# Performance work log

Hardware: AMD Instinct MI355X
Metric: run time of the kernel (lower is better)

## Reference

```python
import jax, jax.numpy as jnp
import numpy as np

B, S, C, L = 8, 256, 4, 256
E, H, NL, NS = 256, 8, 2, 8
DH = E // H
EPS = 1e-5


def _conv1d(x, w, b):
    # x: [B, Cin, L], w: [Cout, Cin, K] -> [B, Cout, L] (SAME padding, stride 1)
    y = jax.lax.conv_general_dilated(x, w, (1,), 'SAME', dimension_numbers=('NCH', 'OIH', 'NCH'))
    return y + b[None, :, None]


def _local_cnn(xs, w1, b1, w2, b2):
    # xs: [B, 4, L] for one segment; per-segment weights
    h = jax.nn.relu(_conv1d(xs, w1, b1))
    h = jax.nn.relu(_conv1d(h, w2, b2))
    return jnp.max(h, axis=-1)  # AdaptiveMaxPool1d(1) + squeeze -> [B, E]


def _layernorm(x, g, b):
    m = jnp.mean(x, axis=-1, keepdims=True)
    v = jnp.mean((x - m) ** 2, axis=-1, keepdims=True)
    return (x - m) / jnp.sqrt(v + EPS) * g + b


def setup_inputs() -> dict:
    key = jax.random.key(0)
    ks = jax.random.split(key, 24)
    n = lambda k, shp, s: jax.random.normal(k, shp, jnp.float32) * s
    return {
        'x': jax.random.normal(ks[0], (B, S, C, L), jnp.float32),
        'conv1_w': n(ks[1], (S, 128, 4, 3), 0.1), 'conv1_b': jnp.zeros((S, 128), jnp.float32),
        'conv2_w': n(ks[2], (S, E, 128, 3), 0.05), 'conv2_b': jnp.zeros((S, E), jnp.float32),
        'ln1_g': jnp.ones((NL, E), jnp.float32), 'ln1_b': jnp.zeros((NL, E), jnp.float32),
        'wq': n(ks[3], (NL, E, E), 0.02), 'bq': jnp.zeros((NL, E), jnp.float32),
        'wk': n(ks[4], (NL, E, E), 0.02), 'bk': jnp.zeros((NL, E), jnp.float32),
        'wv': n(ks[5], (NL, E, E), 0.02), 'bv': jnp.zeros((NL, E), jnp.float32),
        'wo': n(ks[6], (NL, E, E), 0.02), 'bo': jnp.zeros((NL, E), jnp.float32),
        'bias_w': n(ks[7], (NL, 4, H), 0.1), 'bias_b': jnp.zeros((NL, H), jnp.float32),
        'ln2_g': jnp.ones((NL, E), jnp.float32), 'ln2_b': jnp.zeros((NL, E), jnp.float32),
        'ffn_w1': n(ks[8], (NL, E, 2 * E), 0.02), 'ffn_b1': jnp.zeros((NL, 2 * E), jnp.float32),
        'ffn_w2': n(ks[9], (NL, 2 * E, E), 0.02), 'ffn_b2': jnp.zeros((NL, E), jnp.float32),
        'fc_w': n(ks[10], (NS * E, 2), 0.02), 'fc_b': jnp.zeros((2,), jnp.float32),
    }


def _forward(x, conv1_w, conv1_b, conv2_w, conv2_b, ln1_g, ln1_b,
             wq, bq, wk, bk, wv, bv, wo, bo, bias_w, bias_b,
             ln2_g, ln2_b, ffn_w1, ffn_b1, ffn_w2, ffn_b2, fc_w, fc_b):
    # Per-segment CNNs (vmap over segment axis with per-segment weights) -> [B, S, E]
    cnn = jax.vmap(_local_cnn, in_axes=(1, 0, 0, 0, 0), out_axes=1)(x, conv1_w, conv1_b, conv2_w, conv2_b)
    feat = _layernorm(cnn, jnp.ones((E,), cnn.dtype), jnp.zeros((E,), cnn.dtype))  # F.layer_norm, no affine

    # bias matrices: cdist (p=2), global-max normalized; positional distance; inverses
    sq = jnp.sum(feat * feat, axis=-1)  # [B, S]
    d2 = sq[:, :, None] + sq[:, None, :] - 2.0 * jnp.einsum('bie,bje->bij', feat, feat)
    dist = jnp.sqrt(jnp.maximum(d2, 0.0))
    dist = dist / (jnp.max(dist) + 1e-6)
    idx = jnp.arange(S, dtype=feat.dtype)
    rdist = jnp.abs(idx[:, None] - idx[None, :]) / (S - 1)
    rdist = jnp.broadcast_to(rdist[None], (feat.shape[0], S, S))
    attn_bias = jnp.stack([dist, rdist, 1.0 - rdist, 1.0 - dist], axis=-1)  # [B,S,S,4]

    h = feat
    scale = 1.0 / jnp.sqrt(jnp.asarray(DH, h.dtype))
    for l in range(NL):
        hn = _layernorm(h, ln1_g[l], ln1_b[l])
        q = (hn @ wq[l] + bq[l]).reshape(-1, S, H, DH)
        k = (hn @ wk[l] + bk[l]).reshape(-1, S, H, DH)
        v = (hn @ wv[l] + bv[l]).reshape(-1, S, H, DH)
        scores = jnp.einsum('bihd,bjhd->bhij', q, k) * scale
        scores = scores + jnp.einsum('bijc,ch->bhij', attn_bias, bias_w[l]) + bias_b[l][None, :, None, None]
        a = jax.nn.softmax(scores, axis=-1)
        o = jnp.einsum('bhij,bjhd->bihd', a, v).reshape(-1, S, E) @ wo[l] + bo[l]
        h = h + o
        hn2 = _layernorm(h, ln2_g[l], ln2_b[l])
        f = jax.nn.relu(hn2 @ ffn_w1[l] + ffn_b1[l]) @ ffn_w2[l] + ffn_b2[l]
        h = h + f

    # split into NS chunks along segments, max-pool each, concat (S % NS == 0)
    pooled = jnp.max(h.reshape(-1, NS, S // NS, E), axis=2).reshape(-1, NS * E)
    return pooled @ fc_w + fc_b  # [B, num_classes]


def reference(x, conv1_w, conv1_b, conv2_w, conv2_b, ln1_g, ln1_b,
              wq, bq, wk, bk, wv, bv, wo, bo, bias_w, bias_b,
              ln2_g, ln2_b, ffn_w1, ffn_b1, ffn_w2, ffn_b2, fc_w, fc_b):
    return _forward(x, conv1_w, conv1_b, conv2_w, conv2_b, ln1_g, ln1_b,
                    wq, bq, wk, bk, wv, bv, wo, bo, bias_w, bias_b,
                    ln2_g, ln2_b, ffn_w1, ffn_b1, ffn_w2, ffn_b2, fc_w, fc_b)
```

## Files before the change

### kernel.cpp

```cpp
#include <hip/hip_runtime.h>
#include <hip/hip_bf16.h>


typedef float floatx4 __attribute__((ext_vector_type(4)));
typedef short bf16x8 __attribute__((ext_vector_type(8)));

__device__ __forceinline__ float wave_sum(float v) {
    v += __shfl_xor(v, 32); v += __shfl_xor(v, 16); v += __shfl_xor(v, 8);
    v += __shfl_xor(v, 4);  v += __shfl_xor(v, 2);  v += __shfl_xor(v, 1);
    return v;
}
__device__ __forceinline__ float wave_max(float v) {
    v = fmaxf(v, __shfl_xor(v, 32)); v = fmaxf(v, __shfl_xor(v, 16));
    v = fmaxf(v, __shfl_xor(v, 8));  v = fmaxf(v, __shfl_xor(v, 4));
    v = fmaxf(v, __shfl_xor(v, 2));  v = fmaxf(v, __shfl_xor(v, 1));
    return v;
}
__device__ __forceinline__ unsigned short f2bf(float v) {
    unsigned b = __float_as_uint(v);
    unsigned r = (b + 0x7fffu + ((b >> 16) & 1u)) >> 16;
    return (unsigned short)r;
}

typedef const __attribute__((address_space(1))) unsigned int* gas_u32p;
typedef __attribute__((address_space(3))) unsigned int* las_u32p;

__device__ __forceinline__ void stage_chunk(const unsigned short* gbase,
                                            unsigned short* lbase,
                                            int wv, int lane)
{
    const char* g = (const char*)gbase + (wv << 11) + (lane << 4);
    char* l = (char*)lbase + (wv << 11);
    __builtin_amdgcn_global_load_lds((gas_u32p)(const void*)g,
                                     (las_u32p)(void*)l, 16, 0, 0);
    __builtin_amdgcn_global_load_lds((gas_u32p)(const void*)(g + 1024),
                                     (las_u32p)(void*)(l + 1024), 16, 0, 0);
}

__global__ __launch_bounds__(256) void prep_all_kernel(
    unsigned* __restrict__ dmax, unsigned* __restrict__ cnnmax,
    const float* __restrict__ wq, const float* __restrict__ wk,
    const float* __restrict__ wv, const float* __restrict__ wo,
    const float* __restrict__ f1, const float* __restrict__ f2,
    unsigned short* __restrict__ wtb,
    const float* __restrict__ w2, unsigned short* __restrict__ w2b)
{
    __shared__ float t[32][33];
    const int bid = blockIdx.x;
    const int tid = threadIdx.x;

    if (bid < 2048) {
        const size_t i = (size_t)bid * 256 + tid;
        cnnmax[i] = 0u;
        if (i == 0) *dmax = 0u;
        return;
    }
    if (bid < 5120) {
        const int idx = bid - 2048;
        const int z = idx >> 8;
        const int by = (idx >> 4) & 15;
        const int bx = idx & 15;
        const int l = z / 6, id = z % 6;
        const float* src; int K_, N_; size_t doff;
        switch (id) {
            case 0:  src = wq + (size_t)l * 65536;  K_ = 256; N_ = 256; doff = 0;      break;
            case 1:  src = wk + (size_t)l * 65536;  K_ = 256; N_ = 256; doff = 65536;  break;
            case 2:  src = wv + (size_t)l * 65536;  K_ = 256; N_ = 256; doff = 131072; break;
            case 3:  src = wo + (size_t)l * 65536;  K_ = 256; N_ = 256; doff = 196608; break;
            case 4:  src = f1 + (size_t)l * 131072; K_ = 256; N_ = 512; doff = 262144; break;
            default: src = f2 + (size_t)l * 131072; K_ = 512; N_ = 256; doff = 393216; break;
        }
        const int k0 = bx * 32, n0 = by * 32;
        if (k0 >= K_ || n0 >= N_) return;
        unsigned short* dst = wtb + (size_t)l * 524288 + doff;
        const int c = tid & 31, rq = tid >> 5;
#pragma unroll
        for (int i = 0; i < 4; i++) {
            const int r = rq + i * 8;
            t[r][c] = src[(size_t)(k0 + r) * N_ + n0 + c];
        }
        __syncthreads();
#pragma unroll
        for (int i = 0; i < 4; i++) {
            const int r = rq + i * 8;
            dst[(size_t)(n0 + r) * K_ + k0 + c] = f2bf(t[c][r]);
        }
        return;
    }
    {
        const int idx = bid - 5120;
        const int s = idx & 255;
        const int part = idx >> 8;
        const float* src = w2 + (size_t)s * 98304;
        unsigned short* dst = w2b + (size_t)s * 98304;
        for (int o = part * 24576 + tid; o < (part + 1) * 24576; o += 256) {
            const int c  = o >> 13;
            const int w  = o & 8191;
            const int co = w >> 5;
            const int up = (w >> 3) & 3;
            const int tt = w & 7;
            const int u  = (up ^ co ^ (co >> 2)) & 3;
            const int kk = c * 32 + u * 8 + tt;
            const int ci = kk & 127, tap = kk >> 7;
            dst[o] = f2bf(src[(size_t)co * 384 + ci * 3 + tap]);
        }
    }
}

__global__ __launch_bounds__(512, 4) void conv2_fused_kernel(
    const unsigned short* __restrict__ w2b,
    const float* __restrict__ x,
    const float* __restrict__ w1,
    const float* __restrict__ b1,
    const float* __restrict__ b2,
    unsigned* __restrict__ cnnmax)
{
    __shared__ float xs[4][258];
    __shared__ float w1s[1536];
    __shared__ unsigned short Hs[130 * 136];
    __shared__ unsigned short Ab[2][8192];

    const int tid = threadIdx.x;
    const int lane = tid & 63;
    const int wv = __builtin_amdgcn_readfirstlane((int)(tid >> 6));
    const int wm = wv & 3, wn = wv >> 2;
    const int bid = blockIdx.x;
    const int xcd = bid & 7;
    const int pos = bid >> 3;
    const int s   = xcd * 32 + (pos >> 4);
    const int nt  = pos & 15;
    const int b = nt >> 1;
    const int l0 = (nt & 1) * 128;
    const int lr = lane & 15;
    const int quad = lane >> 4;
    const int qk = quad * 8;

    const float* xp = x + ((size_t)(b * 256 + s)) * 1024;
    for (int i = tid; i < 1024; i += 512) {
        const int ci = i >> 8, l = i & 255;
        xs[ci][l + 1] = xp[i];
    }
    if (tid < 4) { xs[tid][0] = 0.f; xs[tid][257] = 0.f; }
    const float* w1p = w1 + (size_t)s * 1536;
    for (int i = tid; i < 1536; i += 512) w1s[i] = w1p[i];
    const int co1 = tid & 127;
    const float bb1 = b1[s * 128 + co1];
    __syncthreads();

    const unsigned short* wchunks = w2b + (size_t)s * 98304;
    stage_chunk(wchunks, &Ab[0][0], wv, lane);

    {
        const int g = tid >> 7;
        float wreg[12];
#pragma unroll
        for (int k = 0; k < 12; k++) wreg[k] = w1s[co1 * 12 + k];
        for (int pr = g; pr < 130; pr += 4) {
            const int l = l0 - 1 + pr;
            float a = 0.f;
            if ((unsigned)l < 256u) {
                a = bb1;
#pragma unroll
                for (int ci = 0; ci < 4; ci++)
#pragma unroll
                    for (int k = 0; k < 3; k++) a = fmaf(wreg[ci * 3 + k], xs[ci][l + k], a);
                a = fmaxf(a, 0.f);
            }
            Hs[pr * 136 + co1] = f2bf(a);
        }
    }

    floatx4 acc[4][4];
#pragma unroll
    for (int r = 0; r < 4; r++)
#pragma unroll
        for (int c = 0; c < 4; c++) acc[r][c] = (floatx4){0.f, 0.f, 0.f, 0.f};

    const int nb = wn * 64;
    const int aoff = wm * 2048 + lr * 32 + (((quad ^ lr ^ (lr >> 2)) & 3) * 8);
    const int hbase = (nb + lr) * 136 + qk;

    asm volatile("s_waitcnt vmcnt(0) lgkmcnt(0)" ::: "memory");
    __builtin_amdgcn_s_barrier();
    __builtin_amdgcn_sched_barrier(0);

#pragma unroll
    for (int ks = 0; ks < 12; ks++) {
        if (ks) {
            asm volatile("s_waitcnt vmcnt(0)" ::: "memory");
            __builtin_amdgcn_s_barrier();
            __builtin_amdgcn_sched_barrier(0);
        }
        if (ks < 11)
            stage_chunk(wchunks + (size_t)(ks + 1) * 8192, &Ab[(ks + 1) & 1][0], wv, lane);
        const int tap_ = ks >> 2, ci0_ = (ks & 3) * 32;
        const unsigned short* ap = &Ab[ks & 1][aoff];
        const unsigned short* hp = &Hs[hbase + tap_ * 136 + ci0_];
        bf16x8 a[4], bb[4];
#pragma unroll
        for (int r = 0; r < 4; r++) a[r] = *(const bf16x8*)(ap + r * 512);
#pragma unroll
        for (int c = 0; c < 4; c++) bb[c] = *(const bf16x8*)(hp + c * 2176);
#pragma unroll
        for (int r = 0; r < 4; r++)
#pragma unroll
            for (int c = 0; c < 4; c++)
                acc[r][c] = __builtin_amdgcn_mfma_f32_16x16x32_bf16(
                    a[r], bb[c], acc[r][c], 0, 0, 0);
    }

    const float* b2s = b2 + s * 256;
    unsigned* cmrow = cnnmax + ((size_t)(b * 256 + s)) * 256;
#pragma unroll
    for (int r = 0; r < 4; r++) {
#pragma unroll
        for (int e = 0; e < 4; e++) {
            const int co = wm * 64 + r * 16 + quad * 4 + e;
            const float bias = b2s[co];
            float mv = 0.f;
#pragma unroll
            for (int c = 0; c < 4; c++) mv = fmaxf(mv, acc[r][c][e] + bias);
            mv = fmaxf(mv, __shfl_xor(mv, 1));
            mv = fmaxf(mv, __shfl_xor(mv, 2));
            mv = fmaxf(mv, __shfl_xor(mv, 4));
            mv = fmaxf(mv, __shfl_xor(mv, 8));
            if (lr == 0) atomicMax(&cmrow[co], __float_as_uint(mv));
        }
    }
}

__global__ __launch_bounds__(256) void ln0_kernel(
    const unsigned* __restrict__ cm, float* __restrict__ out, float* __restrict__ sqv)
{
    const int tid = threadIdx.x, lane = tid & 63, wid = tid >> 6;
    const int row = blockIdx.x * 4 + wid;
    const unsigned* xr = cm + (size_t)row * 256;
    float v[4];
#pragma unroll
    for (int i = 0; i < 4; i++) v[i] = __uint_as_float(xr[lane + 64 * i]);
    float sm = wave_sum(v[0] + v[1] + v[2] + v[3]);
    const float mean = sm * (1.f / 256.f);
    float qv = 0.f;
#pragma unroll
    for (int i = 0; i < 4; i++) { const float d = v[i] - mean; qv = fmaf(d, d, qv); }
    qv = wave_sum(qv);
    const float inv = rsqrtf(qv * (1.f / 256.f) + 1e-5f);
    float* orow = out + (size_t)row * 256;
#pragma unroll
    for (int i = 0; i < 4; i++) orow[lane + 64 * i] = (v[i] - mean) * inv;
    if (lane == 0) sqv[row] = qv * inv * inv;
}

__global__ __launch_bounds__(256) void dist_kernel(
    const float* __restrict__ feat, const float* __restrict__ sq,
    float* __restrict__ dist, unsigned* __restrict__ dmax)
{
    __shared__ float Fi[32][260];
    __shared__ float Fj[16][260];
    __shared__ float redm[4];
    const int tid = threadIdx.x;
    const int bid = blockIdx.x;
    const int b = bid >> 7, it = (bid >> 4) & 7, jt = bid & 15;
    const float* fb = feat + (size_t)b * 65536;
    for (int idx = tid; idx < 32 * 256; idx += 256) {
        const int r = idx >> 8, e = idx & 255;
        Fi[r][e] = fb[(it * 32 + r) * 256 + e];
    }
    for (int idx = tid; idx < 16 * 256; idx += 256) {
        const int r = idx >> 8, e = idx & 255;
        Fj[r][e] = fb[(jt * 16 + r) * 256 + e];
    }
    __syncthreads();
    const int ii = tid >> 3, j0 = (tid & 7) * 2;
    float acc[2] = {0.f, 0.f};
    for (int e = 0; e < 256; e += 4) {
        const float4 a = *(const float4*)&Fi[ii][e];
#pragma unroll
        for (int u = 0; u < 2; u++) {
            const float4 bv = *(const float4*)&Fj[j0 + u][e];
            acc[u] += a.x * bv.x + a.y * bv.y + a.z * bv.z + a.w * bv.w;
        }
    }
    const float sqi = sq[b * 256 + it * 32 + ii];
    float mymax = 0.f;
#pragma unroll
    for (int u = 0; u < 2; u++) {
        const float d2 = sqi + sq[b * 256 + jt * 16 + j0 + u] - 2.f * acc[u];
        const float d = sqrtf(fmaxf(d2, 0.f));
        dist[((size_t)b * 256 + it * 32 + ii) * 256 + jt * 16 + j0 + u] = d;
        mymax = fmaxf(mymax, d);
    }
    mymax = wave_max(mymax);
    if ((tid & 63) == 0) redm[tid >> 6] = mymax;
    __syncthreads();
    if (tid == 0) {
        const float m = fmaxf(fmaxf(redm[0], redm[1]), fmaxf(redm[2], redm[3]));
        atomicMax(dmax, __float_as_uint(m));
    }
}

__global__ __launch_bounds__(128) void gemm_ln_kernel(
    const float* __restrict__ hf, const unsigned short* __restrict__ Wt,
    const float* __restrict__ g, const float* __restrict__ bta,
    const float* __restrict__ b0, const float* __restrict__ b1, const float* __restrict__ b2,
    unsigned short* __restrict__ o0, unsigned short* __restrict__ o1, unsigned short* __restrict__ o2,
    int mode)
{
    __shared__ unsigned short As[64 * 264];
    const int tid = threadIdx.x;
    const int lane = tid & 63, lr = lane & 15, quad = lane >> 4;
    const int wv = __builtin_amdgcn_readfirstlane((int)(tid >> 6));
    const int m0 = blockIdx.x * 64;
    const int n0 = blockIdx.y * 32;

    {
        const int g16 = lane >> 4, l16 = lane & 15;
        const int c0 = l16 * 16;
        float4 g4[4], bt4[4];
#pragma unroll
        for (int k = 0; k < 4; k++) {
            g4[k]  = *(const float4*)&g[c0 + 4 * k];
            bt4[k] = *(const float4*)&bta[c0 + 4 * k];
        }
#pragma unroll
        for (int pass = 0; pass < 8; pass++) {
            const int row = wv * 32 + pass * 4 + g16;
            const float* hr = hf + (size_t)(m0 + row) * 256 + c0;
            float4 v[4];
#pragma unroll
            for (int k = 0; k < 4; k++) v[k] = *(const float4*)&hr[4 * k];
            float s = 0.f;
#pragma unroll
            for (int k = 0; k < 4; k++) s += v[k].x + v[k].y + v[k].z + v[k].w;
            s += __shfl_xor(s, 1); s += __shfl_xor(s, 2);
            s += __shfl_xor(s, 4); s += __shfl_xor(s, 8);
            const float mean = s * (1.f / 256.f);
            float q = 0.f;
#pragma unroll
            for (int k = 0; k < 4; k++) {
                float d;
                d = v[k].x - mean; q = fmaf(d, d, q);
                d = v[k].y - mean; q = fmaf(d, d, q);
                d = v[k].z - mean; q = fmaf(d, d, q);
                d = v[k].w - mean; q = fmaf(d, d, q);
            }
            q += __shfl_xor(q, 1); q += __shfl_xor(q, 2);
            q += __shfl_xor(q, 4); q += __shfl_xor(q, 8);
            const float inv = rsqrtf(q * (1.f / 256.f) + 1e-5f);
            unsigned* dst = (unsigned*)&As[row * 264 + c0];
#pragma unroll
            for (int k = 0; k < 4; k++) {
                const float f0 = (v[k].x - mean) * inv * g4[k].x + bt4[k].x;
                const float f1 = (v[k].y - mean) * inv * g4[k].y + bt4[k].y;
                const float f2 = (v[k].z - mean) * inv * g4[k].z + bt4[k].z;
                const float f3 = (v[k].w - mean) * inv * g4[k].w + bt4[k].w;
                dst[2 * k]     = (unsigned)f2bf(f0) | ((unsigned)f2bf(f1) << 16);
                dst[2 * k + 1] = (unsigned)f2bf(f2) | ((unsigned)f2bf(f3) << 16);
            }
        }
    }
    __syncthreads();

    floatx4 acc[2][2];
#pragma unroll
    for (int r = 0; r < 2; r++)
#pragma unroll
        for (int c = 0; c < 2; c++) acc[r][c] = (floatx4){0.f, 0.f, 0.f, 0.f};

    const unsigned short* Ap = &As[(wv * 32 + lr) * 264 + quad * 8];
    const unsigned short* Bp = Wt + (size_t)(n0 + lr) * 256 + quad * 8;
#pragma unroll
    for (int ks = 0; ks < 8; ks++) {
        const int ko = ks * 32;
        bf16x8 a[2], b[2];
#pragma unroll
        for (int r = 0; r < 2; r++) a[r] = *(const bf16x8*)(Ap + r * 16 * 264 + ko);
#pragma unroll
        for (int c = 0; c < 2; c++) b[c] = *(const bf16x8*)(Bp + (size_t)c * 16 * 256 + ko);
#pragma unroll
        for (int r = 0; r < 2; r++)
#pragma unroll
            for (int c = 0; c < 2; c++)
                acc[r][c] = __builtin_amdgcn_mfma_f32_16x16x32_bf16(a[r], b[c], acc[r][c], 0, 0, 0);
    }

    const int mw0 = m0 + wv * 32;
    if (mode == 0) {
        const int which = n0 >> 8, nn0 = n0 & 255;
        if (which < 2) {
            unsigned short* op = which ? o1 : o0;
            const float* bp = which ? b1 : b0;
#pragma unroll
            for (int r = 0; r < 2; r++)
#pragma unroll
                for (int c = 0; c < 2; c++)
#pragma unroll
                    for (int e = 0; e < 4; e++) {
                        const int m = mw0 + r * 16 + quad * 4 + e;
                        const int n = nn0 + c * 16 + lr;
                        op[(size_t)m * 256 + n] = f2bf(acc[r][c][e] + bp[n]);
                    }
        } else {
#pragma unroll
            for (int r = 0; r < 2; r++)
#pragma unroll
                for (int c = 0; c < 2; c++)
#pragma unroll
                    for (int e = 0; e < 4; e++) {
                        const int m = mw0 + r * 16 + quad * 4 + e;
                        const int nn = nn0 + c * 16 + lr;
                        const int bb_ = m >> 8, j = m & 255, hh = nn >> 5, d = nn & 31;
                        o2[(size_t)((bb_ * 8 + hh) * 32 + d) * 256 + j] = f2bf(acc[r][c][e] + b2[nn]);
                    }
        }
    } else {
#pragma unroll
        for (int r = 0; r < 2; r++)
#pragma unroll
            for (int c = 0; c < 2; c++)
#pragma unroll
                for (int e = 0; e < 4; e++) {
                    const int m = mw0 + r * 16 + quad * 4 + e;
                    const int n = n0 + c * 16 + lr;
                    o0[(size_t)m * 512 + n] = f2bf(fmaxf(acc[r][c][e] + b0[n], 0.f));
                }
    }
}

__global__ __launch_bounds__(128) void gemm_mfma_kernel(
    const unsigned short* __restrict__ A, const unsigned short* __restrict__ Wt,
    const float* __restrict__ b0, const float* __restrict__ b1, const float* __restrict__ b2,
    const float* __restrict__ R, float* __restrict__ outf,
    unsigned short* __restrict__ o0, unsigned short* __restrict__ o1, unsigned short* __restrict__ o2,
    int K, int mode)
{
    const int tid = threadIdx.x;
    const int lane = tid & 63, lr = lane & 15, quad = lane >> 4;
    const int wv = __builtin_amdgcn_readfirstlane((int)(tid >> 6));
    const int m0 = blockIdx.x * 64 + wv * 32;
    const int n0 = blockIdx.y * 32;

    floatx4 acc[2][2];
#pragma unroll
    for (int r = 0; r < 2; r++)
#pragma unroll
        for (int c = 0; c < 2; c++) acc[r][c] = (floatx4){0.f, 0.f, 0.f, 0.f};

    const unsigned short* Ap = A + (size_t)(m0 + lr) * K + quad * 8;
    const unsigned short* Bp = Wt + (size_t)(n0 + lr) * K + quad * 8;
    const int nks = K >> 5;
#pragma unroll 4
    for (int ks = 0; ks < nks; ks++) {
        const int ko = ks * 32;
        bf16x8 a[2], b[2];
#pragma unroll
        for (int r = 0; r < 2; r++) a[r] = *(const bf16x8*)(Ap + (size_t)r * 16 * K + ko);
#pragma unroll
        for (int c = 0; c < 2; c++) b[c] = *(const bf16x8*)(Bp + (size_t)c * 16 * K + ko);
#pragma unroll
        for (int r = 0; r < 2; r++)
#pragma unroll
            for (int c = 0; c < 2; c++)
                acc[r][c] = __builtin_amdgcn_mfma_f32_16x16x32_bf16(a[r], b[c], acc[r][c], 0, 0, 0);
    }

    if (mode == 0) {
        const int which = n0 >> 8, nn0 = n0 & 255;
        if (which < 2) {
            unsigned short* op = which ? o1 : o0;
            const float* bp = which ? b1 : b0;
#pragma unroll
            for (int r = 0; r < 2; r++)
#pragma unroll
                for (int c = 0; c < 2; c++)
#pragma unroll
                    for (int e = 0; e < 4; e++) {
                        const int m = m0 + r * 16 + quad * 4 + e;
                        const int n = nn0 + c * 16 + lr;
                        op[(size_t)m * 256 + n] = f2bf(acc[r][c][e] + bp[n]);
                    }
        } else {
#pragma unroll
            for (int r = 0; r < 2; r++)
#pragma unroll
                for (int c = 0; c < 2; c++)
#pragma unroll
                    for (int e = 0; e < 4; e++) {
                        const int m = m0 + r * 16 + quad * 4 + e;
                        const int nn = nn0 + c * 16 + lr;
                        const int bb_ = m >> 8, j = m & 255, hh = nn >> 5, d = nn & 31;
                        o2[(size_t)((bb_ * 8 + hh) * 32 + d) * 256 + j] = f2bf(acc[r][c][e] + b2[nn]);
                    }
        }
    } else if (mode == 1) {
#pragma unroll
        for (int r = 0; r < 2; r++)
#pragma unroll
            for (int c = 0; c < 2; c++)
#pragma unroll
                for (int e = 0; e < 4; e++) {
                    const int m = m0 + r * 16 + quad * 4 + e;
                    const int n = n0 + c * 16 + lr;
                    outf[(size_t)m * 256 + n] = acc[r][c][e] + b0[n] + R[(size_t)m * 256 + n];
                }
    } else {
#pragma unroll
        for (int r = 0; r < 2; r++)
#pragma unroll
            for (int c = 0; c < 2; c++)
#pragma unroll
                for (int e = 0; e < 4; e++) {
                    const int m = m0 + r * 16 + quad * 4 + e;
                    const int n = n0 + c * 16 + lr;
                    o0[(size_t)m * 512 + n] = f2bf(fmaxf(acc[r][c][e] + b0[n], 0.f));
                }
    }
}

__global__ __launch_bounds__(256) void attn_mfma_kernel(
    const unsigned short* __restrict__ q_bf, const unsigned short* __restrict__ k_bf,
    const unsigned short* __restrict__ vt_bf,
    const float* __restrict__ dist, const unsigned* __restrict__ dmax,
    const float* __restrict__ bw, const float* __restrict__ bb,
    unsigned short* __restrict__ ao_bf)
{
    __shared__ unsigned short Ps[4][16][264];
    const int tid = threadIdx.x;
    const int lane = tid & 63, lr = lane & 15, quad = lane >> 4;
    const int wv = __builtin_amdgcn_readfirstlane((int)(tid >> 6));
    const int ic = blockIdx.x, hh = blockIdx.y, b = blockIdx.z;
    const int i0 = ic * 64 + wv * 16;

    const float dinv = 1.f / (__uint_as_float(*dmax) + 1e-6f);
    const float w0 = bw[0 * 8 + hh], w1 = bw[1 * 8 + hh], w2 = bw[2 * 8 + hh], w3 = bw[3 * 8 + hh];
    const float bbh = bb[hh];
    const float scale = 0.17677669529663687f;

    const bf16x8 aq = *(const bf16x8*)(q_bf + (size_t)(b * 256 + i0 + lr) * 256 + hh * 32 + quad * 8);
    floatx4 sc[16];
#pragma unroll
    for (int c = 0; c < 16; c++) {
        const bf16x8 bk = *(const bf16x8*)(k_bf + (size_t)(b * 256 + c * 16 + lr) * 256 + hh * 32 + quad * 8);
        sc[c] = __builtin_amdgcn_mfma_f32_16x16x32_bf16(aq, bk, (floatx4){0.f, 0.f, 0.f, 0.f}, 0, 0, 0);
    }

#pragma unroll
    for (int e = 0; e < 4; e++) {
        const int i = i0 + quad * 4 + e;
        const float* drow = dist + ((size_t)(b * 256 + i)) * 256;
        float bs[16];
        float mx = -1e30f;
#pragma unroll
        for (int c = 0; c < 16; c++) {
            const int j = c * 16 + lr;
            const float dn = drow[j] * dinv;
            const float rd = fabsf((float)(i - j)) * (1.f / 255.f);
            bs[c] = sc[c][e] * scale + w0 * dn + w1 * rd + w2 * (1.f - rd) + w3 * (1.f - dn) + bbh;
            mx = fmaxf(mx, bs[c]);
        }
        mx = fmaxf(mx, __shfl_xor(mx, 1)); mx = fmaxf(mx, __shfl_xor(mx, 2));
        mx = fmaxf(mx, __shfl_xor(mx, 4)); mx = fmaxf(mx, __shfl_xor(mx, 8));
        float sm = 0.f;
#pragma unroll
        for (int c = 0; c < 16; c++) { bs[c] = __expf(bs[c] - mx); sm += bs[c]; }
        sm += __shfl_xor(sm, 1); sm += __shfl_xor(sm, 2);
        sm += __shfl_xor(sm, 4); sm += __shfl_xor(sm, 8);
        const float rs = 1.f / sm;
#pragma unroll
        for (int c = 0; c < 16; c++)
            Ps[wv][quad * 4 + e][c * 16 + lr] = f2bf(bs[c] * rs);
    }
    __syncthreads();

    floatx4 oc[2];
    oc[0] = (floatx4){0.f, 0.f, 0.f, 0.f};
    oc[1] = (floatx4){0.f, 0.f, 0.f, 0.f};
    const unsigned short* vtb = vt_bf + (size_t)(b * 8 + hh) * 8192;
#pragma unroll
    for (int ks = 0; ks < 8; ks++) {
        const bf16x8 ap = *(const bf16x8*)(&Ps[wv][lr][ks * 32 + quad * 8]);
#pragma unroll
        for (int c2 = 0; c2 < 2; c2++) {
            const bf16x8 bvv = *(const bf16x8*)(vtb + (size_t)(c2 * 16 + lr) * 256 + ks * 32 + quad * 8);
            oc[c2] = __builtin_amdgcn_mfma_f32_16x16x32_bf16(ap, bvv, oc[c2], 0, 0, 0);
        }
    }
#pragma unroll
    for (int c2 = 0; c2 < 2; c2++)
#pragma unroll
        for (int e = 0; e < 4; e++)
            ao_bf[(size_t)(b * 256 + i0 + quad * 4 + e) * 256 + hh * 32 + c2 * 16 + lr] = f2bf(oc[c2][e]);
}

__global__ __launch_bounds__(256) void pool_fc_kernel(
    const float* __restrict__ h, const float* __restrict__ fcw,
    const float* __restrict__ fcb, float* __restrict__ out)
{
    __shared__ float red[8];
    const int b = blockIdx.x, tid = threadIdx.x, lane = tid & 63, wid = tid >> 6;
    float a0 = 0.f, a1 = 0.f;
    for (int ns = 0; ns < 8; ns++) {
        const float* hp = h + ((size_t)(b * 256 + ns * 32)) * 256 + tid;
        float m = hp[0];
#pragma unroll
        for (int r = 1; r < 32; r++) m = fmaxf(m, hp[(size_t)r * 256]);
        a0 = fmaf(m, fcw[(ns * 256 + tid) * 2 + 0], a0);
        a1 = fmaf(m, fcw[(ns * 256 + tid) * 2 + 1], a1);
    }
    a0 = wave_sum(a0);
    a1 = wave_sum(a1);
    if (lane == 0) { red[wid] = a0; red[4 + wid] = a1; }
    __syncthreads();
    if (tid == 0) out[b * 2 + 0] = red[0] + red[1] + red[2] + red[3] + fcb[0];
    if (tid == 1) out[b * 2 + 1] = red[4] + red[5] + red[6] + red[7] + fcb[1];
}

extern "C" void kernel_launch(void* const* d_in, const int* in_sizes, int n_in,
                              void* d_out, int out_size, void* d_ws, size_t ws_size,
                              hipStream_t stream)
{
    (void)in_sizes; (void)n_in; (void)out_size; (void)ws_size;
    const float* x       = (const float*)d_in[0];
    const float* conv1_w = (const float*)d_in[1];
    const float* conv1_b = (const float*)d_in[2];
    const float* conv2_w = (const float*)d_in[3];
    const float* conv2_b = (const float*)d_in[4];
    const float* ln1_g   = (const float*)d_in[5];
    const float* ln1_b   = (const float*)d_in[6];
    const float* wq = (const float*)d_in[7];  const float* bq = (const float*)d_in[8];
    const float* wk = (const float*)d_in[9];  const float* bk = (const float*)d_in[10];
    const float* wvp = (const float*)d_in[11]; const float* bv = (const float*)d_in[12];
    const float* wo = (const float*)d_in[13]; const float* bo = (const float*)d_in[14];
    const float* bias_w = (const float*)d_in[15];
    const float* bias_b = (const float*)d_in[16];
    const float* ln2_g  = (const float*)d_in[17];
    const float* ln2_b  = (const float*)d_in[18];
    const float* ffn_w1 = (const float*)d_in[19]; const float* ffn_b1 = (const float*)d_in[20];
    const float* ffn_w2 = (const float*)d_in[21]; const float* ffn_b2 = (const float*)d_in[22];
    const float* fc_w   = (const float*)d_in[23]; const float* fc_b = (const float*)d_in[24];
    float* out = (float*)d_out;

    float* ws = (float*)d_ws;
    float* h    = ws;
    float* dist = h + 524288;
    float* sqv  = dist + 524288;
    unsigned* dmax = (unsigned*)(sqv + 2048);
    unsigned* cnnmax = (unsigned*)(sqv + 2048 + 16);
    unsigned short* hn_bf = (unsigned short*)(sqv + 2048 + 16 + 524288);
    unsigned short* q_bf  = hn_bf + 524288;
    unsigned short* k_bf  = q_bf + 524288;
    unsigned short* vt_bf = k_bf + 524288;
    unsigned short* ao_bf = vt_bf + 524288;
    unsigned short* fm_bf = ao_bf + 524288;
    unsigned short* wtb   = fm_bf + 1048576;
    unsigned short* w2b   = wtb + 1048576;

    prep_all_kernel<<<6144, 256, 0, stream>>>(
        dmax, cnnmax, wq, wk, wvp, wo, ffn_w1, ffn_w2, wtb, conv2_w, w2b);
    conv2_fused_kernel<<<4096, 512, 0, stream>>>(
        w2b, x, conv1_w, conv1_b, conv2_b, cnnmax);
    ln0_kernel<<<512, 256, 0, stream>>>(cnnmax, h, sqv);
    dist_kernel<<<1024, 256, 0, stream>>>(h, sqv, dist, dmax);

    for (int l = 0; l < 2; l++) {
        const unsigned short* wqkvT = wtb + (size_t)l * 524288;
        const unsigned short* woT   = wqkvT + 196608;
        const unsigned short* f1T   = wqkvT + 262144;
        const unsigned short* f2T   = wqkvT + 393216;

        gemm_ln_kernel<<<dim3(32, 24), 128, 0, stream>>>(
            h, wqkvT, ln1_g + l * 256, ln1_b + l * 256,
            bq + l * 256, bk + l * 256, bv + l * 256,
            q_bf, k_bf, vt_bf, 0);
        attn_mfma_kernel<<<dim3(4, 8, 8), 256, 0, stream>>>(
            q_bf, k_bf, vt_bf, dist, dmax, bias_w + l * 32, bias_b + l * 8, ao_bf);
        gemm_mfma_kernel<<<dim3(32, 8), 128, 0, stream>>>(
            ao_bf, woT, bo + l * 256, nullptr, nullptr,
            h, h, nullptr, nullptr, nullptr, 256, 1);
        gemm_ln_kernel<<<dim3(32, 16), 128, 0, stream>>>(
            h, f1T, ln2_g + l * 256, ln2_b + l * 256,
            ffn_b1 + l * 512, nullptr, nullptr,
            fm_bf, nullptr, nullptr, 2);
        gemm_mfma_kernel<<<dim3(32, 8), 128, 0, stream>>>(
            fm_bf, f2T, ffn_b2 + l * 256, nullptr, nullptr,
            h, h, nullptr, nullptr, nullptr, 512, 1);
    }
    pool_fc_kernel<<<8, 256, 0, stream>>>(h, fc_w, fc_b, out);
}
```

Measured before the change: 571.9 us.

## Vectorize conv2 weight prep, pack conv1 outputs in pairs, split pool-fc across segments

The conv2 weight conversion now reads float4s coalesced from the source and scatters them to the swizzled bf16 layout through a per-block LDS index table, instead of doing a gathered scalar read per output element. Conv1 in the fused kernel now computes two output channels per thread with packed 2-wide FMAs and writes both bf16 values in one 32-bit store. The pool_fc kernel is spread over 64 blocks, one per batch and chunk, and accumulates into the output with atomicAdd. The output is pre-initialised with the fc bias inside the prep kernel. This adds float atomics, so the summation order is no longer deterministic.

Measured after the change: 575.3 us. Within noise of the previous version (+0.6%).

```diff
diff --git a/kernel.cpp b/kernel.cpp
--- a/kernel.cpp
+++ b/kernel.cpp
@@ -3,6 +3,7 @@
 
 
 typedef float floatx4 __attribute__((ext_vector_type(4)));
+typedef float f32x2 __attribute__((ext_vector_type(2)));
 typedef short bf16x8 __attribute__((ext_vector_type(8)));
 
 __device__ __forceinline__ float wave_sum(float v) {
@@ -43,9 +44,11 @@
     const float* __restrict__ wv, const float* __restrict__ wo,
     const float* __restrict__ f1, const float* __restrict__ f2,
     unsigned short* __restrict__ wtb,
-    const float* __restrict__ w2, unsigned short* __restrict__ w2b)
+    const float* __restrict__ w2, unsigned short* __restrict__ w2b,
+    const float* __restrict__ fcb, float* __restrict__ outbuf)
 {
     __shared__ float t[32][33];
+    __shared__ unsigned tbl[1536];
     const int bid = blockIdx.x;
     const int tid = threadIdx.x;
 
@@ -53,6 +56,7 @@
         const size_t i = (size_t)bid * 256 + tid;
         cnnmax[i] = 0u;
         if (i == 0) *dmax = 0u;
+        if (bid == 0 && tid < 16) outbuf[tid] = fcb[tid & 1];
         return;
     }
     if (bid < 5120) {
@@ -91,18 +95,29 @@
         const int idx = bid - 5120;
         const int s = idx & 255;
         const int part = idx >> 8;
-        const float* src = w2 + (size_t)s * 98304;
+        for (int i = tid; i < 1536; i += 256) {
+            const int sw = i / 384, j = i - sw * 384;
+            const int ci = (j * 21846) >> 16;
+            const int tap = j - ci * 3;
+            const int kk = tap * 128 + ci;
+            const int c = kk >> 5, rel = kk & 31;
+            const int u = rel >> 3, tt = rel & 7;
+            tbl[i] = (unsigned)(c * 8192 + (((u ^ sw) & 3) << 3) + tt);
+        }
+        __syncthreads();
+        const float4* src4 = (const float4*)(w2 + (size_t)s * 98304);
         unsigned short* dst = w2b + (size_t)s * 98304;
-        for (int o = part * 24576 + tid; o < (part + 1) * 24576; o += 256) {
-            const int c  = o >> 13;
-            const int w  = o & 8191;
-            const int co = w >> 5;
-            const int up = (w >> 3) & 3;
-            const int tt = w & 7;
-            const int u  = (up ^ co ^ (co >> 2)) & 3;
-            const int kk = c * 32 + u * 8 + tt;
-            const int ci = kk & 127, tap = kk >> 7;
-            dst[o] = f2bf(src[(size_t)co * 384 + ci * 3 + tap]);
+        for (int q = part * 6144 + tid; q < (part + 1) * 6144; q += 256) {
+            const int co = (((q >> 5) * 21846) >> 16);
+            const int j0 = (q - co * 96) * 4;
+            const int sw = (co ^ (co >> 2)) & 3;
+            const unsigned* tb = &tbl[sw * 384 + j0];
+            const float4 v = src4[q];
+            const int base = co * 32;
+            dst[tb[0] + base] = f2bf(v.x);
+            dst[tb[1] + base] = f2bf(v.y);
+            dst[tb[2] + base] = f2bf(v.z);
+            dst[tb[3] + base] = f2bf(v.w);
         }
     }
 }
@@ -143,30 +158,35 @@
     if (tid < 4) { xs[tid][0] = 0.f; xs[tid][257] = 0.f; }
     const float* w1p = w1 + (size_t)s * 1536;
     for (int i = tid; i < 1536; i += 512) w1s[i] = w1p[i];
-    const int co1 = tid & 127;
-    const float bb1 = b1[s * 128 + co1];
+    const int co2 = (tid & 63) * 2;
+    const f32x2 bb2 = {b1[s * 128 + co2], b1[s * 128 + co2 + 1]};
     __syncthreads();
 
     const unsigned short* wchunks = w2b + (size_t)s * 98304;
     stage_chunk(wchunks, &Ab[0][0], wv, lane);
 
     {
-        const int g = tid >> 7;
-        float wreg[12];
-#pragma unroll
-        for (int k = 0; k < 12; k++) wreg[k] = w1s[co1 * 12 + k];
-        for (int pr = g; pr < 130; pr += 4) {
+        const int g8 = tid >> 6;
+        f32x2 wreg[12];
+#pragma unroll
+        for (int k = 0; k < 12; k++)
+            wreg[k] = (f32x2){w1s[co2 * 12 + k], w1s[co2 * 12 + 12 + k]};
+        for (int pr = g8; pr < 130; pr += 8) {
             const int l = l0 - 1 + pr;
-            float a = 0.f;
+            unsigned pk = 0u;
             if ((unsigned)l < 256u) {
-                a = bb1;
+                f32x2 a2 = bb2;
 #pragma unroll
                 for (int ci = 0; ci < 4; ci++)
 #pragma unroll
-                    for (int k = 0; k < 3; k++) a = fmaf(wreg[ci * 3 + k], xs[ci][l + k], a);
-                a = fmaxf(a, 0.f);
+                    for (int k = 0; k < 3; k++) {
+                        const float xv = xs[ci][l + k];
+                        a2 = __builtin_elementwise_fma(wreg[ci * 3 + k], (f32x2){xv, xv}, a2);
+                    }
+                a2 = __builtin_elementwise_max(a2, (f32x2){0.f, 0.f});
+                pk = (unsigned)f2bf(a2.x) | ((unsigned)f2bf(a2.y) << 16);
             }
-            Hs[pr * 136 + co1] = f2bf(a);
+            *(unsigned*)&Hs[pr * 136 + co2] = pk;
         }
     }
 
@@ -594,25 +614,23 @@
 
 __global__ __launch_bounds__(256) void pool_fc_kernel(
     const float* __restrict__ h, const float* __restrict__ fcw,
-    const float* __restrict__ fcb, float* __restrict__ out)
+    float* __restrict__ out)
 {
     __shared__ float red[8];
-    const int b = blockIdx.x, tid = threadIdx.x, lane = tid & 63, wid = tid >> 6;
-    float a0 = 0.f, a1 = 0.f;
-    for (int ns = 0; ns < 8; ns++) {
-        const float* hp = h + ((size_t)(b * 256 + ns * 32)) * 256 + tid;
-        float m = hp[0];
-#pragma unroll
-        for (int r = 1; r < 32; r++) m = fmaxf(m, hp[(size_t)r * 256]);
-        a0 = fmaf(m, fcw[(ns * 256 + tid) * 2 + 0], a0);
-        a1 = fmaf(m, fcw[(ns * 256 + tid) * 2 + 1], a1);
-    }
+    const int b = blockIdx.x, ns = blockIdx.y;
+    const int tid = threadIdx.x, lane = tid & 63, wid = tid >> 6;
+    const float* hp = h + ((size_t)(b * 256 + ns * 32)) * 256 + tid;
+    float m = hp[0];
+#pragma unroll
+    for (int r = 1; r < 32; r++) m = fmaxf(m, hp[(size_t)r * 256]);
+    float a0 = m * fcw[(ns * 256 + tid) * 2 + 0];
+    float a1 = m * fcw[(ns * 256 + tid) * 2 + 1];
     a0 = wave_sum(a0);
     a1 = wave_sum(a1);
     if (lane == 0) { red[wid] = a0; red[4 + wid] = a1; }
     __syncthreads();
-    if (tid == 0) out[b * 2 + 0] = red[0] + red[1] + red[2] + red[3] + fcb[0];
-    if (tid == 1) out[b * 2 + 1] = red[4] + red[5] + red[6] + red[7] + fcb[1];
+    if (tid == 0) atomicAdd(&out[b * 2 + 0], red[0] + red[1] + red[2] + red[3]);
+    if (tid == 1) atomicAdd(&out[b * 2 + 1], red[4] + red[5] + red[6] + red[7]);
 }
 
 extern "C" void kernel_launch(void* const* d_in, const int* in_sizes, int n_in,
@@ -656,7 +674,8 @@
     unsigned short* w2b   = wtb + 1048576;
 
     prep_all_kernel<<<6144, 256, 0, stream>>>(
-        dmax, cnnmax, wq, wk, wvp, wo, ffn_w1, ffn_w2, wtb, conv2_w, w2b);
+        dmax, cnnmax, wq, wk, wvp, wo, ffn_w1, ffn_w2, wtb, conv2_w, w2b,
+        fc_b, out);
     conv2_fused_kernel<<<4096, 512, 0, stream>>>(
         w2b, x, conv1_w, conv1_b, conv2_b, cnnmax);
     ln0_kernel<<<512, 256, 0, stream>>>(cnnmax, h, sqv);
@@ -685,5 +704,5 @@
             fm_bf, f2T, ffn_b2 + l * 256, nullptr, nullptr,
             h, h, nullptr, nullptr, nullptr, 512, 1);
     }
-    pool_fc_kernel<<<8, 256, 0, stream>>>(h, fc_w, fc_b, out);
-}
+    pool_fc_kernel<<<dim3(8, 8), 256, 0, stream>>>(h, fc_w, out);
+}
```
